# Performance work log

Hardware: AMD Instinct MI355X
Metric: run time of the kernel (lower is better)

The kernel has to match this reference:

```python
import jax, jax.numpy as jnp
import numpy as np

TOP_K = 32
EPS = 1e-12  # matches torch F.normalize eps


def _l2_normalize(v, axis):
    n = jnp.linalg.norm(v, axis=axis, keepdims=True)
    return v / jnp.maximum(n, EPS)


def setup_inputs() -> dict:
    key = jax.random.key(0)
    k1, k2, k3 = jax.random.split(key, 3)
    x = jax.random.normal(k1, (2, 1024, 1024), dtype=jnp.float32)
    weight = jax.random.normal(k2, (50257, 1024), dtype=jnp.float32) * 0.02
    bias = jax.random.normal(k3, (50257,), dtype=jnp.float32) * 0.02
    return {"x": x, "weight": weight, "bias": bias}


def reference(x, weight, bias):
    out_dim, in_dim = weight.shape
    # precomputed in torch __init__: row-normalized routing table
    weight_norm = _l2_normalize(weight, axis=1)            # [O, I]
    x_flat = x.reshape(-1, in_dim)                          # [N, I]
    x_norm = _l2_normalize(x_flat, axis=1)                  # [N, I]
    logits = x_norm @ weight_norm.T                         # [N, O] cosine sims
    _, topk_ids = jax.lax.top_k(logits, TOP_K)              # [N, K]
    # batched gather of weight rows, per-token matvec, scatter into sparse out
    w_topk = weight[topk_ids]                               # [N, K, I]
    local = jnp.einsum('nki,ni->nk', w_topk, x_flat)        # [N, K]
    local = local + bias[topk_ids]
    n = x_flat.shape[0]
    out = jnp.zeros((n, out_dim), dtype=x.dtype)
    out = out.at[jnp.arange(n)[:, None], topk_ids].set(local)
    return out.reshape(*x.shape[:-1], out_dim)
```

## Files before the change

kernel.cpp:

```cpp
#include <hip/hip_runtime.h>

#define NTOK 2048
#define DIM  1024
#define OUTD 50257
#define OPAD 50304
#define NCB  393
#define SEGC 12
#define TOPK 32
#define RCAP 256
#define NREF 80
#define THRESH 0.08f
#define NBLK 6288

typedef float f32x4 __attribute__((ext_vector_type(4)));

__device__ __forceinline__ unsigned int f2e4m3(float f){
    unsigned int u = __float_as_uint(f);
    unsigned int sgn = (u >> 24) & 0x80u;
    int exp = (int)((u >> 23) & 0xFF);
    unsigned int man = u & 0x7FFFFF;
    int e = exp - 127;
    if (e >= 9) return sgn | 0x7E;
    unsigned int full = 0x800000u | man;
    int shift = (e >= -6) ? 20 : 20 + (-6 - e);
    if (shift >= 24) return sgn;
    unsigned int kept = full >> shift;
    unsigned int rem  = full & ((1u << shift) - 1);
    unsigned int half = 1u << (shift - 1);
    if (rem > half || (rem == half && (kept & 1))) kept++;
    if (e >= -6){
        unsigned int ee = (unsigned)(e + 7);
        if (kept >= 16){ kept >>= 1; ee++; }
        if (ee > 15 || (ee == 15 && (kept & 7) > 6)) return sgn | 0x7E;
        return sgn | (ee << 3) | (kept - 8);
    } else {
        if (kept >= 8) return sgn | 0x08;
        return sgn | kept;
    }
}
__device__ __forceinline__ unsigned int pack4_e4m3(float a, float b, float c, float d){
    return f2e4m3(a) | (f2e4m3(b) << 8) | (f2e4m3(c) << 16) | (f2e4m3(d) << 24);
}

#define GLDS(gp, lp) __builtin_amdgcn_global_load_lds( \
    (__attribute__((address_space(1))) void*)(gp),     \
    (__attribute__((address_space(3))) void*)(lp), 16, 0, 0)

extern "C" __global__ void k_init(const float* __restrict__ x,
                                  unsigned char* __restrict__ x8){
    __shared__ double ls[4];
    const int row = blockIdx.x, t = threadIdx.x;
    float4 v = ((const float4*)(x + (size_t)row * DIM))[t];
    double s = (double)v.x*v.x + (double)v.y*v.y
             + (double)v.z*v.z + (double)v.w*v.w;
    for (int d = 32; d >= 1; d >>= 1) s += __shfl_xor(s, d, 64);
    const int wv = t >> 6, ln = t & 63;
    if (ln == 0) ls[wv] = s;
    __syncthreads();
    double tot = ls[0] + ls[1] + ls[2] + ls[3];
    float sc = (float)(32.0 / fmax(sqrt(tot), 1e-12));
    ((unsigned int*)(x8 + (size_t)row * DIM))[t] =
        pack4_e4m3(v.x*sc, v.y*sc, v.z*sc, v.w*sc);
}

extern "C" __global__ void k_wnorm(const float* __restrict__ w,
                                   unsigned char* __restrict__ w8,
                                   double* __restrict__ ri64){
    __shared__ double ls[4];
    int r = blockIdx.x, t = threadIdx.x;
    if (r < OUTD){
        float4 v = ((const float4*)(w + (size_t)r * DIM))[t];
        double s = (double)v.x*v.x + (double)v.y*v.y
                 + (double)v.z*v.z + (double)v.w*v.w;
        for (int d = 32; d >= 1; d >>= 1) s += __shfl_xor(s, d, 64);
        int wv = t >> 6, ln = t & 63;
        if (ln == 0) ls[wv] = s;
        __syncthreads();
        double tot = ls[0] + ls[1] + ls[2] + ls[3];
        double ri = 1.0 / fmax(sqrt(tot), 1e-12);
        if (t == 0) ri64[r] = ri;
        float sc = (float)(32.0 * ri);
        ((unsigned int*)(w8 + (size_t)r * DIM))[t] =
            pack4_e4m3(v.x*sc, v.y*sc, v.z*sc, v.w*sc);
    } else {
        ((unsigned int*)(w8 + (size_t)r * DIM))[t] = 0u;
        if (t == 0) ri64[r] = 0.0;
    }
}

#define COMPUTE(b) do { \
  long af_[4], bv_[4]; \
  const char* Ab_ = As[b] + (lk>>1)*2048 + (lk&1)*8; \
  const char* Bb_ = Bs[b] + (lk>>1)*2048 + (lk&1)*8; \
  _Pragma("unroll") \
  for (int m_ = 0; m_ < 4; ++m_) \
    af_[m_] = *(const long*)(Ab_ + (wm*64 + m_*16 + lr)*16); \
  _Pragma("unroll") \
  for (int n_ = 0; n_ < 4; ++n_) \
    bv_[n_] = *(const long*)(Bb_ + (wn*64 + n_*16 + lr)*16); \
  __builtin_amdgcn_s_setprio(1); \
  _Pragma("unroll") \
  for (int m_ = 0; m_ < 4; ++m_) \
    _Pragma("unroll") \
    for (int n_ = 0; n_ < 4; ++n_) \
      acc[m_][n_] = __builtin_amdgcn_mfma_f32_16x16x32_fp8_fp8( \
                        af_[m_], bv_[n_], acc[m_][n_], 0, 0, 0); \
  __builtin_amdgcn_s_setprio(0); \
} while(0)

#define STAGE(b, K0) do { \
  GLDS(x8 + offA + (K0), As[b] + dstOff); \
  GLDS(w8 + offB + (K0), Bs[b] + dstOff); \
} while(0)

extern "C" __global__ __launch_bounds__(256)
void k_gemm(const unsigned char* __restrict__ x8,
            const unsigned char* __restrict__ w8,
            unsigned long long* __restrict__ cpk,
            unsigned char* __restrict__ cnt8,
            float* __restrict__ out){
    __shared__ __align__(16) char As[2][4096];
    __shared__ __align__(16) char Bs[2][4096];
    __shared__ int lcnt[128];
    const int tid = threadIdx.x;

    const int orig  = blockIdx.x;
    const int newid = (orig & 7) * 786 + (orig >> 3);
    const int bm    = (newid & 15) * 128;
    const int cb    = newid >> 4;
    const int bn    = cb * 128;

    const int wv = tid >> 6, lane = tid & 63;
    const int wm = wv >> 1,  wn = wv & 1;
    const int lr = lane & 15, lk = lane >> 4;

    if (tid < 128) lcnt[tid] = 0;

    f32x4 z = {0.f, 0.f, 0.f, 0.f};
    f32x4 acc[4][4];
    for (int m = 0; m < 4; ++m) for (int n = 0; n < 4; ++n) acc[m][n] = z;

    const int srow   = tid & 127;
    const int sh     = tid >> 7;
    const int dstOff = sh*2048 + srow*16;
    const size_t offA = (size_t)(bm + srow)*DIM + sh*16;
    const size_t offB = (size_t)(bn + srow)*DIM + sh*16;

    const size_t n4 = (size_t)NTOK * OUTD / 4;
    const float4 z4 = make_float4(0.f, 0.f, 0.f, 0.f);

    STAGE(0, 0);
    __syncthreads();
    int buf = 0, it = 0;
    for (int k0 = 32; k0 < DIM; k0 += 32){
        STAGE(buf ^ 1, k0);
        if (it < 16){
            size_t zi = ((size_t)orig*16 + it)*256 + tid;
            if (zi < n4) ((float4*)out)[zi] = z4;
        }
        COMPUTE(buf);
        __syncthreads();
        buf ^= 1; ++it;
    }
    COMPUTE(buf);

    const float inv = 1.0f / 1024.0f;
    #pragma unroll
    for (int n = 0; n < 4; ++n){
        int gcol = bn + wn*64 + n*16 + lr;
        bool ok = gcol < OUTD;
        #pragma unroll
        for (int m = 0; m < 4; ++m){
            int lr0 = wm*64 + m*16 + lk*4;
            #pragma unroll
            for (int r = 0; r < 4; ++r){
                float sc = acc[m][n][r] * inv;
                if (ok && sc > THRESH){
                    int lrow = lr0 + r;
                    int pos = atomicAdd(&lcnt[lrow], 1);
                    if (pos < SEGC)
                        cpk[((size_t)(bm + lrow)*NCB + cb)*SEGC + pos] =
                            ((unsigned long long)(unsigned)gcol << 32) |
                            (unsigned long long)__float_as_uint(sc);
                }
            }
        }
    }
    __syncthreads();
    if (tid < 128)
        cnt8[(size_t)(bm + tid)*NCB + cb] =
            (unsigned char)min(lcnt[tid], SEGC);
}

extern "C" __global__ __launch_bounds__(256)
void k_sel(const float* __restrict__ x, const float* __restrict__ w,
           const float* __restrict__ bias,
           const unsigned long long* __restrict__ cpk,
           const unsigned char* __restrict__ cnt8,
           const double* __restrict__ ri64,
           float* __restrict__ out){
    const int row = blockIdx.x, tid = threadIdx.x;
    __shared__ float  xl[DIM];
    __shared__ int    hist[256];
    __shared__ int    bstar, nref;
    __shared__ int    ridx[RCAP];
    __shared__ double rsc[RCAP];
    __shared__ double rdv[RCAP];

    ((float4*)xl)[tid] = ((const float4*)(x + (size_t)row*DIM))[tid];
    hist[tid] = 0;
    if (tid == 0) nref = 0;
    __syncthreads();

    const unsigned char* rc8 = cnt8 + (size_t)row*NCB;
    const unsigned long long* rseg = cpk + (size_t)row*NCB*SEGC;

    for (int cb = tid; cb < NCB; cb += 256){
        int c = rc8[cb];
        for (int j = 0; j < c; ++j){
            float s = __uint_as_float((unsigned)(rseg[cb*SEGC + j] & 0xFFFFFFFFu));
            int b = (int)((s - THRESH) * 1280.f);
            b = max(0, min(255, b));
            atomicAdd(&hist[b], 1);
        }
    }
    __syncthreads();
    if (tid == 0){
        int cum = 0, b = 255;
        for (; b >= 0; --b){ cum += hist[b]; if (cum >= NREF) break; }
        bstar = b < 0 ? 0 : b;
    }
    __syncthreads();
    const int bs_ = bstar;
    for (int cb = tid; cb < NCB; cb += 256){
        int c = rc8[cb];
        for (int j = 0; j < c; ++j){
            unsigned long long pk = rseg[cb*SEGC + j];
            float s = __uint_as_float((unsigned)(pk & 0xFFFFFFFFu));
            int b = (int)((s - THRESH) * 1280.f);
            b = max(0, min(255, b));
            if (b >= bs_){
                int p = atomicAdd(&nref, 1);
                if (p < RCAP) ridx[p] = (int)(pk >> 32);
            }
        }
    }
    __syncthreads();
    const int nr = min(nref, RCAP);

    const int wv = tid >> 6, lane = tid & 63;
    const float4* xl4 = (const float4*)xl;
    for (int q = wv; q < nr; q += 4){
        int col = ridx[q];
        const float4* wr4 = (const float4*)(w + (size_t)col*DIM);
        double s = 0.0;
        #pragma unroll
        for (int u = 0; u < 4; ++u){
            float4 a = xl4[lane + 64*u];
            float4 b = wr4[lane + 64*u];
            s = fma((double)a.x, (double)b.x, s);
            s = fma((double)a.y, (double)b.y, s);
            s = fma((double)a.z, (double)b.z, s);
            s = fma((double)a.w, (double)b.w, s);
        }
        for (int d = 32; d >= 1; d >>= 1) s += __shfl_xor(s, d, 64);
        if (lane == 0){ rdv[q] = s; rsc[q] = s * ri64[col]; }
    }
    __syncthreads();
    if (tid >= nr){ rsc[tid] = -1.0e300; ridx[tid] = 0x7FFFFFFF; rdv[tid] = 0.0; }
    __syncthreads();

    for (int k = 2; k <= RCAP; k <<= 1){
        for (int j = k >> 1; j > 0; j >>= 1){
            int i = tid, ixj = i ^ j;
            if (ixj > i){
                double sa = rsc[i], sb = rsc[ixj];
                int ia = ridx[i], ib = ridx[ixj];
                bool dir = ((i & k) == 0);
                bool pb = (sb > sa) || (sb == sa && ib < ia);
                if (pb == dir){
                    rsc[i] = sb; rsc[ixj] = sa;
                    ridx[i] = ib; ridx[ixj] = ia;
                    double t = rdv[i]; rdv[i] = rdv[ixj]; rdv[ixj] = t;
                }
            }
            __syncthreads();
        }
    }
    if (tid < TOPK && tid < nr){
        int col = ridx[tid];
        out[(size_t)row*OUTD + col] = (float)rdv[tid] + bias[col];
    }
}

extern "C" void kernel_launch(void* const* d_in, const int* in_sizes, int n_in,
                              void* d_out, int out_size, void* d_ws, size_t ws_size,
                              hipStream_t stream){
    const float* x    = (const float*)d_in[0];
    const float* wgt  = (const float*)d_in[1];
    const float* bias = (const float*)d_in[2];
    float* out = (float*)d_out;
    char* ws = (char*)d_ws;

    unsigned char* w8 = (unsigned char*)ws;
    unsigned char* x8 = (unsigned char*)(ws + 51511296);
    double* ri64 = (double*)(ws + 53608448);
    unsigned long long* cpk = (unsigned long long*)(ws + 54010880);
    unsigned char* cnt8 = (unsigned char*)(ws + 131277824);

    k_init <<<NTOK, 256, 0, stream>>>(x, x8);
    k_wnorm<<<OPAD, 256, 0, stream>>>(wgt, w8, ri64);
    k_gemm <<<NBLK, 256, 0, stream>>>(x8, w8, cpk, cnt8, out);
    k_sel  <<<NTOK, 256, 0, stream>>>(x, wgt, bias, cpk, cnt8, ri64, out);
}
```

Measured before the change: 529.6 us.

## Enlarge FP8 GEMM tile to 256x128 with 512 threads and relax barrier waits

The FP8 cosine-similarity GEMM block now covers 256 token rows instead of 128, using 8 waves (512 threads), so each loaded weight tile is reused across twice as many rows. The grid is halved and the shared-memory A buffer, staging indices, per-row counters and output zeroing stride are resized to match. During the iterations that also zero the output, the full barrier is replaced by a barrier that waits for all but one outstanding memory operation, so the zeroing store need not complete before the barrier. Out-of-range zeroing indices are clamped rather than branched on. The larger block raises register and LDS use per block, which may reduce occupancy.

```diff
diff --git a/kernel.cpp b/kernel.cpp
--- a/kernel.cpp
+++ b/kernel.cpp
@@ -10,7 +10,7 @@
 #define RCAP 256
 #define NREF 80
 #define THRESH 0.08f
-#define NBLK 6288
+#define NBLK 3144
 
 typedef float f32x4 __attribute__((ext_vector_type(4)));
 
@@ -90,7 +90,7 @@
 
 #define COMPUTE(b) do { \
   long af_[4], bv_[4]; \
-  const char* Ab_ = As[b] + (lk>>1)*2048 + (lk&1)*8; \
+  const char* Ab_ = As[b] + (lk>>1)*4096 + (lk&1)*8; \
   const char* Bb_ = Bs[b] + (lk>>1)*2048 + (lk&1)*8; \
   _Pragma("unroll") \
   for (int m_ = 0; m_ < 4; ++m_) \
@@ -109,42 +109,49 @@
 } while(0)
 
 #define STAGE(b, K0) do { \
-  GLDS(x8 + offA + (K0), As[b] + dstOff); \
-  GLDS(w8 + offB + (K0), Bs[b] + dstOff); \
+  GLDS(x8 + offA + (K0), As[b] + dstA); \
+  if (tid < 256) GLDS(w8 + offB + (K0), Bs[b] + dstB); \
 } while(0)
 
-extern "C" __global__ __launch_bounds__(256)
+#define VBARZ() do { \
+  asm volatile("s_waitcnt vmcnt(1)" ::: "memory"); \
+  __builtin_amdgcn_s_barrier(); \
+  asm volatile("" ::: "memory"); \
+} while(0)
+
+extern "C" __global__ __launch_bounds__(512)
 void k_gemm(const unsigned char* __restrict__ x8,
             const unsigned char* __restrict__ w8,
             unsigned long long* __restrict__ cpk,
             unsigned char* __restrict__ cnt8,
             float* __restrict__ out){
-    __shared__ __align__(16) char As[2][4096];
+    __shared__ __align__(16) char As[2][8192];
     __shared__ __align__(16) char Bs[2][4096];
-    __shared__ int lcnt[128];
+    __shared__ int lcnt[256];
     const int tid = threadIdx.x;
 
     const int orig  = blockIdx.x;
-    const int newid = (orig & 7) * 786 + (orig >> 3);
-    const int bm    = (newid & 15) * 128;
-    const int cb    = newid >> 4;
+    const int newid = (orig & 7) * 393 + (orig >> 3);
+    const int bm    = (newid & 7) * 256;
+    const int cb    = newid >> 3;
     const int bn    = cb * 128;
 
     const int wv = tid >> 6, lane = tid & 63;
     const int wm = wv >> 1,  wn = wv & 1;
     const int lr = lane & 15, lk = lane >> 4;
 
-    if (tid < 128) lcnt[tid] = 0;
+    if (tid < 256) lcnt[tid] = 0;
 
     f32x4 z = {0.f, 0.f, 0.f, 0.f};
     f32x4 acc[4][4];
     for (int m = 0; m < 4; ++m) for (int n = 0; n < 4; ++n) acc[m][n] = z;
 
-    const int srow   = tid & 127;
-    const int sh     = tid >> 7;
-    const int dstOff = sh*2048 + srow*16;
-    const size_t offA = (size_t)(bm + srow)*DIM + sh*16;
-    const size_t offB = (size_t)(bn + srow)*DIM + sh*16;
+    const int rowA = tid & 255,        shA = tid >> 8;
+    const int dstA = shA*4096 + rowA*16;
+    const size_t offA = (size_t)(bm + rowA)*DIM + shA*16;
+    const int rowB = tid & 127,        shB = (tid >> 7) & 1;
+    const int dstB = shB*2048 + rowB*16;
+    const size_t offB = (size_t)(bn + rowB)*DIM + shB*16;
 
     const size_t n4 = (size_t)NTOK * OUTD / 4;
     const float4 z4 = make_float4(0.f, 0.f, 0.f, 0.f);
@@ -152,15 +159,17 @@
     STAGE(0, 0);
     __syncthreads();
     int buf = 0, it = 0;
-    for (int k0 = 32; k0 < DIM; k0 += 32){
+    for (int k0 = 32; k0 < DIM; k0 += 32, ++it){
         STAGE(buf ^ 1, k0);
         if (it < 16){
-            size_t zi = ((size_t)orig*16 + it)*256 + tid;
-            if (zi < n4) ((float4*)out)[zi] = z4;
+            size_t zi = ((size_t)orig*16 + it)*512 + tid;
+            if (zi >= n4) zi = n4 - 1;
+            ((float4*)out)[zi] = z4;
         }
         COMPUTE(buf);
-        __syncthreads();
-        buf ^= 1; ++it;
+        if (it < 16) VBARZ();
+        else        __syncthreads();
+        buf ^= 1;
     }
     COMPUTE(buf);
 
@@ -187,7 +196,7 @@
         }
     }
     __syncthreads();
-    if (tid < 128)
+    if (tid < 256)
         cnt8[(size_t)(bm + tid)*NCB + cb] =
             (unsigned char)min(lcnt[tid], SEGC);
 }
@@ -310,6 +319,6 @@
 
     k_init <<<NTOK, 256, 0, stream>>>(x, x8);
     k_wnorm<<<OPAD, 256, 0, stream>>>(wgt, w8, ri64);
-    k_gemm <<<NBLK, 256, 0, stream>>>(x8, w8, cpk, cnt8, out);
+    k_gemm <<<NBLK, 512, 0, stream>>>(x8, w8, cpk, cnt8, out);
     k_sel  <<<NTOK, 256, 0, stream>>>(x, wgt, bias, cpk, cnt8, ri64, out);
 }
```

Measured after the change: 548.6 us. +3.6%, slower.

## Triple-buffer GEMM K-loop with 64-wide k-steps and vmcnt-based barriers

Applied to the files above, without the earlier changes.

Doubles the K-tile from 32 to 64 bytes per stage and moves from a double-buffered LDS pipeline to a triple-buffered one with two loads in flight. Each wait is an explicit s_waitcnt vmcnt(N) plus a raw barrier instead of __syncthreads, so the compute on one buffer overlaps outstanding global-to-LDS loads for the next two. The output zeroing store is folded into each iteration with its index clamped rather than skipped, which removes a branch. The cost is three times the LDS footprint (48KB), which may lower occupancy, and the hand-counted vmcnt values must match the exact number of memory operations issued.

```diff
diff --git a/kernel.cpp b/kernel.cpp
--- a/kernel.cpp
+++ b/kernel.cpp
@@ -89,28 +89,50 @@
 }
 
 #define COMPUTE(b) do { \
-  long af_[4], bv_[4]; \
-  const char* Ab_ = As[b] + (lk>>1)*2048 + (lk&1)*8; \
-  const char* Bb_ = Bs[b] + (lk>>1)*2048 + (lk&1)*8; \
   _Pragma("unroll") \
-  for (int m_ = 0; m_ < 4; ++m_) \
-    af_[m_] = *(const long*)(Ab_ + (wm*64 + m_*16 + lr)*16); \
-  _Pragma("unroll") \
-  for (int n_ = 0; n_ < 4; ++n_) \
-    bv_[n_] = *(const long*)(Bb_ + (wn*64 + n_*16 + lr)*16); \
-  __builtin_amdgcn_s_setprio(1); \
-  _Pragma("unroll") \
-  for (int m_ = 0; m_ < 4; ++m_) \
+  for (int ks_ = 0; ks_ < 2; ++ks_){ \
+    long af_[4], bv_[4]; \
+    const char* Ab_ = As[b] + (ks_*2 + (lk>>1))*2048 + (lk&1)*8; \
+    const char* Bb_ = Bs[b] + (ks_*2 + (lk>>1))*2048 + (lk&1)*8; \
+    _Pragma("unroll") \
+    for (int m_ = 0; m_ < 4; ++m_) \
+      af_[m_] = *(const long*)(Ab_ + (wm*64 + m_*16 + lr)*16); \
     _Pragma("unroll") \
     for (int n_ = 0; n_ < 4; ++n_) \
-      acc[m_][n_] = __builtin_amdgcn_mfma_f32_16x16x32_fp8_fp8( \
-                        af_[m_], bv_[n_], acc[m_][n_], 0, 0, 0); \
-  __builtin_amdgcn_s_setprio(0); \
+      bv_[n_] = *(const long*)(Bb_ + (wn*64 + n_*16 + lr)*16); \
+    __builtin_amdgcn_s_setprio(1); \
+    _Pragma("unroll") \
+    for (int m_ = 0; m_ < 4; ++m_) \
+      _Pragma("unroll") \
+      for (int n_ = 0; n_ < 4; ++n_) \
+        acc[m_][n_] = __builtin_amdgcn_mfma_f32_16x16x32_fp8_fp8( \
+                          af_[m_], bv_[n_], acc[m_][n_], 0, 0, 0); \
+    __builtin_amdgcn_s_setprio(0); \
+  } \
 } while(0)
 
 #define STAGE(b, K0) do { \
-  GLDS(x8 + offA + (K0), As[b] + dstOff); \
-  GLDS(w8 + offB + (K0), Bs[b] + dstOff); \
+  GLDS(x8 + offA0 + (K0), As[b] + tid*16); \
+  GLDS(x8 + offA0 + 32 + (K0), As[b] + (tid+256)*16); \
+  GLDS(w8 + offB0 + (K0), Bs[b] + tid*16); \
+  GLDS(w8 + offB0 + 32 + (K0), Bs[b] + (tid+256)*16); \
+} while(0)
+
+#define ZSTORE(IT) do { \
+  size_t zi_ = ((size_t)orig*16 + (IT))*256 + tid; \
+  if (zi_ >= n4) zi_ = n4 - 1;      \
+  ((float4*)out)[zi_] = z4; \
+} while(0)
+
+#define VBL(N) do { \
+  asm volatile("s_waitcnt vmcnt(" #N ") lgkmcnt(0)" ::: "memory"); \
+  __builtin_amdgcn_s_barrier(); \
+  asm volatile("" ::: "memory"); \
+} while(0)
+
+#define EBAR() do { \
+  __builtin_amdgcn_s_barrier(); \
+  asm volatile("" ::: "memory"); \
 } while(0)
 
 extern "C" __global__ __launch_bounds__(256)
@@ -119,8 +141,8 @@
             unsigned long long* __restrict__ cpk,
             unsigned char* __restrict__ cnt8,
             float* __restrict__ out){
-    __shared__ __align__(16) char As[2][4096];
-    __shared__ __align__(16) char Bs[2][4096];
+    __shared__ __align__(16) char As[3][8192];
+    __shared__ __align__(16) char Bs[3][8192];
     __shared__ int lcnt[128];
     const int tid = threadIdx.x;
 
@@ -140,29 +162,30 @@
     f32x4 acc[4][4];
     for (int m = 0; m < 4; ++m) for (int n = 0; n < 4; ++n) acc[m][n] = z;
 
-    const int srow   = tid & 127;
-    const int sh     = tid >> 7;
-    const int dstOff = sh*2048 + srow*16;
-    const size_t offA = (size_t)(bm + srow)*DIM + sh*16;
-    const size_t offB = (size_t)(bn + srow)*DIM + sh*16;
+    const size_t offA0 = (size_t)(bm + (tid & 127))*DIM + (tid >> 7)*16;
+    const size_t offB0 = (size_t)(bn + (tid & 127))*DIM + (tid >> 7)*16;
 
     const size_t n4 = (size_t)NTOK * OUTD / 4;
     const float4 z4 = make_float4(0.f, 0.f, 0.f, 0.f);
 
     STAGE(0, 0);
-    __syncthreads();
-    int buf = 0, it = 0;
-    for (int k0 = 32; k0 < DIM; k0 += 32){
-        STAGE(buf ^ 1, k0);
-        if (it < 16){
-            size_t zi = ((size_t)orig*16 + it)*256 + tid;
-            if (zi < n4) ((float4*)out)[zi] = z4;
-        }
-        COMPUTE(buf);
-        __syncthreads();
-        buf ^= 1; ++it;
-    }
-    COMPUTE(buf);
+    STAGE(1, 64);
+    STAGE(2, 128); ZSTORE(0);  VBL(9);  COMPUTE(0); EBAR();
+    STAGE(0, 192); ZSTORE(1);  VBL(10); COMPUTE(1); EBAR();
+    {
+        int bufS = 1, bufC = 2;
+        for (int t = 2; t <= 13; ++t){
+            STAGE(bufS, (t+2)*64);
+            ZSTORE(t);
+            VBL(11);
+            COMPUTE(bufC);
+            EBAR();
+            bufS = (bufS == 2) ? 0 : bufS + 1;
+            bufC = (bufC == 2) ? 0 : bufC + 1;
+        }
+    }
+    ZSTORE(14); VBL(7); COMPUTE(2); EBAR();
+    ZSTORE(15); VBL(3); COMPUTE(0);
 
     const float inv = 1.0f / 1024.0f;
     #pragma unroll
```

Result: no change. 526.4 us (-0.6%).
